# Kernel optimization log

Measured on AMD Instinct MI355X. Metric: run time of the kernel, lower is better.

Reference implementation:

```python
import jax, jax.numpy as jnp
import numpy as np

EPS = 1e-6
DIAG_SIZE = 128  # triu band half-width (init kwarg diag_size)
NEG_INF = -1e9


def feature_map(x):
    # tanh feature map: phi(x) = tanh(x) + 1 (positive feature map)
    return jnp.tanh(x) + 1.0


def causal_dot_product(Q, K, V):
    # Q,K: [N,L,H,E], V: [N,L,H,D]
    # running KV state: S_l = sum_{s<=l} K_s V_s^T, materialized via cumsum
    kv = jnp.cumsum(jnp.einsum('nlhe,nlhd->nlhed', K, V), axis=1)  # [N,L,H,E,D]
    return jnp.einsum('nlhe,nlhed->nlhd', Q, kv)


def setup_inputs() -> dict:
    key = jax.random.key(0)
    k1, k2, k3 = jax.random.split(key, 3)
    N, L, H, E = 2, 2048, 8, 64
    queries = jax.random.normal(k1, (N, L, H, E), dtype=jnp.float32)
    keys = jax.random.normal(k2, (N, L, H, E), dtype=jnp.float32)
    values = jax.random.normal(k3, (N, L, H, E), dtype=jnp.float32)
    key_lengths_mask = jnp.ones((N, L), dtype=jnp.float32)  # all keys valid
    blend = jnp.full((1,), 0.9, dtype=jnp.float32)  # learned blend param (init 0.9)
    return {"queries": queries, "keys": keys, "values": values,
            "key_lengths_mask": key_lengths_mask, "blend": blend}


def reference(queries, keys, values, key_lengths_mask, blend):
    N, L, H, E = queries.shape
    # ---- linear attention path (kernel_1 = tanh, kernel_2 = 'none') ----
    Q1 = feature_map(queries)
    K1 = feature_map(keys) * key_lengths_mask[:, :, None, None]
    Z1 = 1.0 / (jnp.einsum('nlhi,nlhi->nlh', Q1, jnp.cumsum(K1, axis=1)) + EPS)
    LV = causal_dot_product(Q1, K1, values) * Z1[..., None]  # [N,L,H,D]
    # ---- full softmax attention path (banded by triu) ----
    softmax_temp = 1.0 / np.sqrt(E).astype(np.float32)
    QK = jnp.einsum('nlhe,nshe->nhls', queries, keys)  # [N,H,L,L]
    l_idx = jnp.arange(L)[:, None]
    s_idx = jnp.arange(L)[None, :]
    causal_add = jnp.where(s_idx <= l_idx, 0.0, NEG_INF)  # lower-triangular mask
    key_add = jnp.where(key_lengths_mask > 0, 0.0, NEG_INF)  # [N,L]
    logits = softmax_temp * (QK + causal_add[None, None] + key_add[:, None, None, :])
    A = jax.nn.softmax(logits, axis=-1)
    # torch.triu(A, diagonal=-diag_size): keep s >= l - diag_size
    band = s_idx >= (l_idx - DIAG_SIZE)
    A = jnp.where(band[None, None], A, 0.0)
    # dropout: eval mode (identity)
    SV = jnp.einsum('nhls,nshd->nlhd', A, values)
    b = blend[0]
    return b * SV + (1.0 - b) * LV
```

## Files before the change

kernel.cpp:

```cpp
#include <hip/hip_runtime.h>
#include <math.h>

#define N_ 2
#define L_ 2048
#define H_ 8
#define E_ 64
#define D_ 64
#define C_ 128
#define NC (L_/C_)
#define ROWSTRIDE (H_*E_)
#define TEMP 0.125f
#define EPS_F 1e-6f
#define NEG_INF_F (-1e9f)
#define CHUNK_WS (E_*D_ + E_)
#define NCHUNKS (N_*H_*NC)
#define TPAD 136
#define PPAD 72

typedef __attribute__((ext_vector_type(8))) short short8;
typedef __attribute__((ext_vector_type(4))) float f32x4;

__device__ __forceinline__ short f2bf(float x) {
  unsigned u = __float_as_uint(x);
  u += 0x7fffu + ((u >> 16) & 1u);
  return (short)(u >> 16);
}
__device__ __forceinline__ float bf2f(short s) {
  return __uint_as_float(((unsigned)(unsigned short)s) << 16);
}
__device__ __forceinline__ float tanh1f(float x) {
  float e = __expf(-2.f * x);
  return 2.f * __builtin_amdgcn_rcpf(1.f + e);
}

__device__ __forceinline__ void load_bf16_tile(short* __restrict__ dst,
                                               const float* __restrict__ src) {
  const int t = threadIdx.x;
#pragma unroll
  for (int it = 0; it < 4; ++it) {
    int gi = it * 256 + t;
    int row = gi >> 3, g = gi & 7;
    const float* p = src + row * ROWSTRIDE + g * 8;
    float4 a = *(const float4*)p;
    float4 b = *(const float4*)(p + 4);
    short8 v;
    v[0] = f2bf(a.x); v[1] = f2bf(a.y); v[2] = f2bf(a.z); v[3] = f2bf(a.w);
    v[4] = f2bf(b.x); v[5] = f2bf(b.y); v[6] = f2bf(b.z); v[7] = f2bf(b.w);
    int sg = g ^ (row & 7);
    *(short8*)(dst + row * 64 + sg * 8) = v;
  }
}

__device__ __forceinline__ short8 frag_ld(const short* __restrict__ buf,
                                          int rowbase, int hf, int lane) {
  int r = rowbase + (lane & 15);
  int g = (hf * 4 + (lane >> 4)) ^ (r & 7);
  return *(const short8*)(buf + r * 64 + g * 8);
}
__device__ __forceinline__ short8 frag_ldT(const short* __restrict__ buf,
                                           int nbase, int g, int lane) {
  int r = nbase + (lane & 15);
  return *(const short8*)(buf + r * TPAD + g * 8);
}
__device__ __forceinline__ short8 frag_ldP(const short* __restrict__ buf,
                                           int rowbase, int ks, int lane) {
  int r = rowbase + (lane & 15);
  int g = ks * 4 + (lane >> 4);
  return *(const short8*)(buf + r * PPAD + g * 8);
}

extern "C" __global__ void __launch_bounds__(256, 4)
k_pre(const float* __restrict__ Q, const float* __restrict__ K,
      const float* __restrict__ V, const float* __restrict__ mask,
      float* __restrict__ ws, float* __restrict__ part) {
  __shared__ short ldsA[64 * TPAD];
  __shared__ short ldsB[64 * TPAD];
  __shared__ float fmsk[C_];
  const int orig = blockIdx.x;
  const int swz = (orig & 7) * 304 + (orig >> 3);
  const int t = threadIdx.x;
  const int w = t >> 6, lane = t & 63;
  const int col_lo = lane & 15;

  if (swz < 2176) {
    const int nh = swz / 136;
    const int p = swz - nh * 136;
    int qb = (int)((sqrtf(8.f * p + 1.f) - 1.f) * 0.5f);
    while ((qb + 1) * (qb + 2) / 2 <= p) ++qb;
    while (qb * (qb + 1) / 2 > p) --qb;
    const int kb = p - qb * (qb + 1) / 2;
    const int h = nh & (H_ - 1), n = nh >> 3;

    load_bf16_tile(ldsA, Q + ((n * L_ + qb * C_) * H_ + h) * E_);
    load_bf16_tile(ldsB, K + ((n * L_ + kb * C_) * H_ + h) * E_);
    if (t < C_) fmsk[t] = mask[n * L_ + kb * C_ + t];
    __syncthreads();

    const int rowbase = w * 32;
    short8 afr[2][2];
#pragma unroll
    for (int m = 0; m < 2; ++m)
#pragma unroll
      for (int hh = 0; hh < 2; ++hh)
        afr[m][hh] = frag_ld(ldsA, rowbase + 16 * m, hh, lane);

    f32x4 acc[2][8];
#pragma unroll
    for (int m = 0; m < 2; ++m)
#pragma unroll
      for (int c = 0; c < 8; ++c) acc[m][c] = (f32x4){0.f, 0.f, 0.f, 0.f};

#pragma unroll
    for (int c = 0; c < 8; ++c) {
      short8 b0 = frag_ld(ldsB, 16 * c, 0, lane);
      short8 b1 = frag_ld(ldsB, 16 * c, 1, lane);
#pragma unroll
      for (int m = 0; m < 2; ++m) {
        acc[m][c] = __builtin_amdgcn_mfma_f32_16x16x32_bf16(afr[m][0], b0, acc[m][c], 0, 0, 0);
        acc[m][c] = __builtin_amdgcn_mfma_f32_16x16x32_bf16(afr[m][1], b1, acc[m][c], 0, 0, 0);
      }
    }

    const bool diag = (kb == qb);
    float* pout = part + (size_t)(nh * NC + qb) * C_ * 16;
#pragma unroll
    for (int m = 0; m < 2; ++m) {
      const int rbase = rowbase + 16 * m + (lane >> 4) * 4;
      float rs[4] = {0.f, 0.f, 0.f, 0.f};
#pragma unroll
      for (int c = 0; c < 8; ++c) {
        const int col = 16 * c + col_lo;
        const float madd = (fmsk[col] > 0.f) ? 0.f : NEG_INF_F;
#pragma unroll
        for (int reg = 0; reg < 4; ++reg) {
          float x = acc[m][c][reg] + madd;
          if (diag && col > rbase + reg) x += NEG_INF_F;
          rs[reg] += __expf(x * TEMP);
        }
      }
#pragma unroll
      for (int off = 1; off < 16; off <<= 1) {
#pragma unroll
        for (int reg = 0; reg < 4; ++reg) rs[reg] += __shfl_xor(rs[reg], off);
      }
      if (col_lo == 0) {
#pragma unroll
        for (int reg = 0; reg < 4; ++reg) pout[(rbase + reg) * 16 + kb] = rs[reg];
      }
    }
  } else {
    const int id = swz - 2176;
    const int nh = id >> 4, c = id & 15;
    const int h = nh & (H_ - 1), n = nh >> 3;
    const int gbase = ((n * L_ + c * C_) * H_ + h) * E_;
    const int e = t & 63, sb = t >> 6;
    const int mbase = n * L_ + c * C_;
#pragma unroll
    for (int q = 0; q < 4; ++q) {
      int s0 = sb * 32 + q * 8;
      short8 kk, vv;
#pragma unroll
      for (int j = 0; j < 8; ++j) {
        float kx = K[gbase + (s0 + j) * ROWSTRIDE + e];
        kk[j] = f2bf(tanh1f(kx) * mask[mbase + s0 + j]);
        vv[j] = f2bf(V[gbase + (s0 + j) * ROWSTRIDE + e]);
      }
      *(short8*)(ldsA + e * TPAD + (s0 >> 3) * 8) = kk;
      *(short8*)(ldsB + e * TPAD + (s0 >> 3) * 8) = vv;
    }
    __syncthreads();

    f32x4 acc[4];
#pragma unroll
    for (int nn = 0; nn < 4; ++nn) acc[nn] = (f32x4){0.f, 0.f, 0.f, 0.f};
#pragma unroll
    for (int ks = 0; ks < 4; ++ks) {
      short8 a = frag_ldT(ldsB, 16 * w, ks * 4 + (lane >> 4), lane);
#pragma unroll
      for (int nn = 0; nn < 4; ++nn) {
        short8 b = frag_ldT(ldsA, 16 * nn, ks * 4 + (lane >> 4), lane);
        acc[nn] = __builtin_amdgcn_mfma_f32_16x16x32_bf16(a, b, acc[nn], 0, 0, 0);
      }
    }
    float* wsc = ws + (size_t)(nh * NC + c) * CHUNK_WS;
    const int drow = 16 * w + ((lane >> 4) << 2);
#pragma unroll
    for (int nn = 0; nn < 4; ++nn)
#pragma unroll
      for (int reg = 0; reg < 4; ++reg)
        wsc[(16 * nn + col_lo) * D_ + drow + reg] = acc[nn][reg];
    if (t < 64) {
      float s = 0.f;
#pragma unroll
      for (int g = 0; g < 16; ++g) {
        short8 v = *(const short8*)(ldsA + t * TPAD + g * 8);
#pragma unroll
        for (int j = 0; j < 8; ++j) s += bf2f(v[j]);
      }
      wsc[E_ * D_ + t] = s;
    }
  }
}

extern "C" __global__ void __launch_bounds__(256)
k_scan(float* __restrict__ ws) {
  const int bid = blockIdx.x;
  const int swz = (bid & 7) * 34 + (bid >> 3);
  const int nh = swz / 17, seg = swz - nh * 17;
  const int idx = seg * 256 + threadIdx.x;
  if (idx >= CHUNK_WS) return;
  float* base = ws + (size_t)nh * NC * CHUNK_WS + idx;
  float v[NC];
#pragma unroll
  for (int c = 0; c < NC; ++c) v[c] = base[(size_t)c * CHUNK_WS];
  float acc = 0.f;
#pragma unroll
  for (int c = 0; c < NC; ++c) {
    base[(size_t)c * CHUNK_WS] = acc;
    acc += v[c];
  }
}

extern "C" __global__ void __launch_bounds__(256, 3)
k_fused(const float* __restrict__ Q, const float* __restrict__ K,
        const float* __restrict__ V, const float* __restrict__ mask,
        const float* __restrict__ blend, const float* __restrict__ ws,
        const float* __restrict__ part, float* __restrict__ out) {
  __shared__ short kbuf[C_ * 64];
  __shared__ short kv[64 * TPAD];
  __shared__ short pbuf[64 * PPAD];
  __shared__ float zlds[64];
  __shared__ float dinv[64];
  __shared__ float ksum[E_];
  __shared__ float kmskC[C_];
  __shared__ float kmskP[C_];

  const int orig = blockIdx.x;
  const int swz = (orig & 7) * 64 + (orig >> 3);
  const int rh = swz & 1, qb = (swz >> 1) & (NC - 1), nh = swz >> 5;
  const int h = nh & (H_ - 1), n = nh >> 3;
  const int t = threadIdx.x;
  const int w = t >> 6, lane = t & 63;
  const int rowbase = w * 16;
  const int col_lo = lane & 15;
  const int rb = rowbase + ((lane >> 4) << 2);
  const int rtile0 = rh * 64 + rb;
  const int qgbase = ((n * L_ + qb * C_ + rh * 64) * H_ + h) * E_;
  const int kbase_chunk = ((n * L_ + qb * C_) * H_ + h) * E_;
  const float* wsc = ws + (size_t)(nh * NC + qb) * CHUNK_WS;
  const float bl = blend[0];
  const float ob = 1.f - bl;
  const int d = t & 63, sb = t >> 6;
  const bool haveprev = (qb > 0);
  const int kgp = ((n * L_ + (qb - 1) * C_) * H_ + h) * E_;

  float4 qraw[2][2];
  {
    const float* qp = Q + qgbase + (rowbase + (lane & 15)) * ROWSTRIDE;
#pragma unroll
    for (int kh = 0; kh < 2; ++kh) {
      int c0 = (kh * 4 + (lane >> 4)) * 8;
      qraw[kh][0] = *(const float4*)(qp + c0);
      qraw[kh][1] = *(const float4*)(qp + c0 + 4);
    }
  }
  short8 kraw[4];
  {
    const float* mrow = mask + n * L_ + qb * C_;
#pragma unroll
    for (int it = 0; it < 4; ++it) {
      int gi = it * 256 + t, row = gi >> 3, g = gi & 7;
      const float* p = K + kbase_chunk + row * ROWSTRIDE + g * 8;
      float4 a = *(const float4*)p, b = *(const float4*)(p + 4);
      float km = mrow[row];
      float xs[8] = {a.x, a.y, a.z, a.w, b.x, b.y, b.z, b.w};
      short8 vr, v1;
#pragma unroll
      for (int j = 0; j < 8; ++j) { vr[j] = f2bf(xs[j]); v1[j] = f2bf(tanh1f(xs[j]) * km); }
      kraw[it] = vr;
      *(short8*)(kbuf + row * 64 + (g ^ (row & 7)) * 8) = v1;
    }
  }
  {
    int eb = t >> 6;
#pragma unroll
    for (int q = 0; q < 2; ++q) {
      int e0 = eb * 16 + q * 8;
      short8 v;
#pragma unroll
      for (int j = 0; j < 8; ++j) v[j] = f2bf(wsc[(e0 + j) * D_ + d]);
      *(short8*)(kv + d * TPAD + (e0 >> 3) * 8) = v;
    }
  }
  short8 vcur[4];
#pragma unroll
  for (int q = 0; q < 4; ++q) {
#pragma unroll
    for (int j = 0; j < 8; ++j)
      vcur[q][j] = f2bf(V[kbase_chunk + (sb * 32 + q * 8 + j) * ROWSTRIDE + d]);
  }
  if (t < 64) {
    ksum[t] = wsc[E_ * D_ + t];
    const float* pb = part + ((size_t)(nh * NC + qb) * C_ + rh * 64 + t) * 16;
    float4 a = *(const float4*)pb, b = *(const float4*)(pb + 4);
    float4 c = *(const float4*)(pb + 8), d4 = *(const float4*)(pb + 12);
    float vv[16] = {a.x, a.y, a.z, a.w, b.x, b.y, b.z, b.w,
                    c.x, c.y, c.z, c.w, d4.x, d4.y, d4.z, d4.w};
    float s = 0.f;
#pragma unroll
    for (int j = 0; j < 16; ++j) s += (j <= qb) ? vv[j] : 0.f;
    dinv[t] = 1.f / s;
  }
  if (t < C_) {
    kmskC[t] = mask[n * L_ + qb * C_ + t];
    kmskP[t] = haveprev ? mask[n * L_ + (qb - 1) * C_ + t] : 1.f;
  }
  __syncthreads();

  short8 af1[2], afs[2];
#pragma unroll
  for (int kh = 0; kh < 2; ++kh) {
    float xs[8] = {qraw[kh][0].x, qraw[kh][0].y, qraw[kh][0].z, qraw[kh][0].w,
                   qraw[kh][1].x, qraw[kh][1].y, qraw[kh][1].z, qraw[kh][1].w};
#pragma unroll
    for (int j = 0; j < 8; ++j) { afs[kh][j] = f2bf(xs[j]); af1[kh][j] = f2bf(tanh1f(xs[j])); }
  }
  f32x4 c1[8];
#pragma unroll
  for (int ct = 0; ct < 8; ++ct) c1[ct] = (f32x4){0.f, 0.f, 0.f, 0.f};
#pragma unroll
  for (int ct = 0; ct < 8; ++ct) {
    short8 b0 = frag_ld(kbuf, 16 * ct, 0, lane);
    short8 b1 = frag_ld(kbuf, 16 * ct, 1, lane);
    c1[ct] = __builtin_amdgcn_mfma_f32_16x16x32_bf16(af1[0], b0, c1[ct], 0, 0, 0);
    c1[ct] = __builtin_amdgcn_mfma_f32_16x16x32_bf16(af1[1], b1, c1[ct], 0, 0, 0);
  }
  {
    float zz = 0.f;
#pragma unroll
    for (int kh = 0; kh < 2; ++kh) {
      int cb = (kh * 4 + (lane >> 4)) * 8;
#pragma unroll
      for (int j = 0; j < 8; ++j) zz += bf2f(af1[kh][j]) * ksum[cb + j];
    }
    zz += __shfl_xor(zz, 16);
    zz += __shfl_xor(zz, 32);
    if (lane < 16) zlds[rowbase + lane] = zz;
  }
  float rs[4] = {0.f, 0.f, 0.f, 0.f};
#pragma unroll
  for (int ct = 0; ct < 8; ++ct) {
    int col = 16 * ct + col_lo;
#pragma unroll
    for (int reg = 0; reg < 4; ++reg) {
      if (col <= rtile0 + reg) rs[reg] += c1[ct][reg];
      else c1[ct][reg] = 0.f;
    }
  }
#pragma unroll
  for (int off = 1; off < 16; off <<= 1)
#pragma unroll
    for (int reg = 0; reg < 4; ++reg) rs[reg] += __shfl_xor(rs[reg], off);

  f32x4 accL[4];
#pragma unroll
  for (int nn = 0; nn < 4; ++nn) accL[nn] = (f32x4){0.f, 0.f, 0.f, 0.f};
#pragma unroll
  for (int ks = 0; ks < 2; ++ks) {
    short8 bf[4];
#pragma unroll
    for (int nn = 0; nn < 4; ++nn)
      bf[nn] = frag_ldT(kv, 16 * nn, ks * 4 + (lane >> 4), lane);
#pragma unroll
    for (int nn = 0; nn < 4; ++nn)
      accL[nn] = __builtin_amdgcn_mfma_f32_16x16x32_bf16(af1[ks], bf[nn], accL[nn], 0, 0, 0);
  }
  __syncthreads();

#pragma unroll
  for (int it = 0; it < 4; ++it) {
    int gi = it * 256 + t, row = gi >> 3, g = gi & 7;
    *(short8*)(kbuf + row * 64 + (g ^ (row & 7)) * 8) = kraw[it];
  }
#pragma unroll
  for (int q = 0; q < 4; ++q)
    *(short8*)(kv + d * TPAD + ((sb * 32 + q * 8) >> 3) * 8) = vcur[q];
  __syncthreads();

  short8 pk[4], pv[4];
  if (haveprev) {
#pragma unroll
    for (int it = 0; it < 4; ++it) {
      int gi = it * 256 + t, row = gi >> 3, g = gi & 7;
      const float* p = K + kgp + row * ROWSTRIDE + g * 8;
      float4 a = *(const float4*)p, b = *(const float4*)(p + 4);
      float xs[8] = {a.x, a.y, a.z, a.w, b.x, b.y, b.z, b.w};
#pragma unroll
      for (int j = 0; j < 8; ++j) pk[it][j] = f2bf(xs[j]);
    }
#pragma unroll
    for (int q = 0; q < 4; ++q)
#pragma unroll
      for (int j = 0; j < 8; ++j)
        pv[q][j] = f2bf(V[kgp + (sb * 32 + q * 8 + j) * ROWSTRIDE + d]);
  }
#pragma unroll
  for (int hh = 0; hh < 2; ++hh) {
#pragma unroll
    for (int ch = 0; ch < 4; ++ch) {
      int ct = 4 * hh + ch, colh = 16 * ch + col_lo;
#pragma unroll
      for (int reg = 0; reg < 4; ++reg)
        pbuf[(rb + reg) * PPAD + colh] = f2bf(c1[ct][reg]);
    }
#pragma unroll
    for (int ks = 0; ks < 2; ++ks) {
      short8 ap = frag_ldP(pbuf, rowbase, ks, lane);
      short8 bv[4];
#pragma unroll
      for (int nn = 0; nn < 4; ++nn)
        bv[nn] = frag_ldT(kv, 16 * nn, 8 * hh + ks * 4 + (lane >> 4), lane);
#pragma unroll
      for (int nn = 0; nn < 4; ++nn)
        accL[nn] = __builtin_amdgcn_mfma_f32_16x16x32_bf16(ap, bv[nn], accL[nn], 0, 0, 0);
    }
  }
  f32x4 accS[4];
#pragma unroll
  for (int nn = 0; nn < 4; ++nn) accS[nn] = (f32x4){0.f, 0.f, 0.f, 0.f};
  {
    f32x4 cs[8];
#pragma unroll
    for (int ct = 0; ct < 8; ++ct) cs[ct] = (f32x4){0.f, 0.f, 0.f, 0.f};
#pragma unroll
    for (int ct = 0; ct < 8; ++ct) {
      short8 b0 = frag_ld(kbuf, 16 * ct, 0, lane);
      short8 b1 = frag_ld(kbuf, 16 * ct, 1, lane);
      cs[ct] = __builtin_amdgcn_mfma_f32_16x16x32_bf16(afs[0], b0, cs[ct], 0, 0, 0);
      cs[ct] = __builtin_amdgcn_mfma_f32_16x16x32_bf16(afs[1], b1, cs[ct], 0, 0, 0);
    }
#pragma unroll
    for (int ct = 0; ct < 8; ++ct) {
      int col = 16 * ct + col_lo;
      float madd = (kmskC[col] > 0.f) ? 0.f : NEG_INF_F;
#pragma unroll
      for (int reg = 0; reg < 4; ++reg) {
        float x = cs[ct][reg] + madd;
        if (col > rtile0 + reg) x += NEG_INF_F;
        cs[ct][reg] = __expf(x * TEMP);
      }
    }
#pragma unroll
    for (int hh = 0; hh < 2; ++hh) {
#pragma unroll
      for (int ch = 0; ch < 4; ++ch) {
        int ct = 4 * hh + ch, colh = 16 * ch + col_lo;
#pragma unroll
        for (int reg = 0; reg < 4; ++reg)
          pbuf[(rb + reg) * PPAD + colh] = f2bf(cs[ct][reg]);
      }
#pragma unroll
      for (int ks = 0; ks < 2; ++ks) {
        short8 ap = frag_ldP(pbuf, rowbase, ks, lane);
        short8 bv[4];
#pragma unroll
        for (int nn = 0; nn < 4; ++nn)
          bv[nn] = frag_ldT(kv, 16 * nn, 8 * hh + ks * 4 + (lane >> 4), lane);
#pragma unroll
        for (int nn = 0; nn < 4; ++nn)
          accS[nn] = __builtin_amdgcn_mfma_f32_16x16x32_bf16(ap, bv[nn], accS[nn], 0, 0, 0);
      }
    }
  }

  if (haveprev) {
    __syncthreads();
#pragma unroll
    for (int it = 0; it < 4; ++it) {
      int gi = it * 256 + t, row = gi >> 3, g = gi & 7;
      *(short8*)(kbuf + row * 64 + (g ^ (row & 7)) * 8) = pk[it];
    }
#pragma unroll
    for (int q = 0; q < 4; ++q)
      *(short8*)(kv + d * TPAD + ((sb * 32 + q * 8) >> 3) * 8) = pv[q];
    __syncthreads();

    f32x4 cs[8];
#pragma unroll
    for (int ct = 0; ct < 8; ++ct) cs[ct] = (f32x4){0.f, 0.f, 0.f, 0.f};
#pragma unroll
    for (int ct = 0; ct < 8; ++ct) {
      short8 b0 = frag_ld(kbuf, 16 * ct, 0, lane);
      short8 b1 = frag_ld(kbuf, 16 * ct, 1, lane);
      cs[ct] = __builtin_amdgcn_mfma_f32_16x16x32_bf16(afs[0], b0, cs[ct], 0, 0, 0);
      cs[ct] = __builtin_amdgcn_mfma_f32_16x16x32_bf16(afs[1], b1, cs[ct], 0, 0, 0);
    }
#pragma unroll
    for (int ct = 0; ct < 8; ++ct) {
      int col = 16 * ct + col_lo;
      float madd = (kmskP[col] > 0.f) ? 0.f : NEG_INF_F;
#pragma unroll
      for (int reg = 0; reg < 4; ++reg) {
        float x = cs[ct][reg] + madd;
        float pp = __expf(x * TEMP);
        if (col < rtile0 + reg) pp = 0.f;
        cs[ct][reg] = pp;
      }
    }
#pragma unroll
    for (int hh = 0; hh < 2; ++hh) {
#pragma unroll
      for (int ch = 0; ch < 4; ++ch) {
        int ct = 4 * hh + ch, colh = 16 * ch + col_lo;
#pragma unroll
        for (int reg = 0; reg < 4; ++reg)
          pbuf[(rb + reg) * PPAD + colh] = f2bf(cs[ct][reg]);
      }
#pragma unroll
      for (int ks = 0; ks < 2; ++ks) {
        short8 ap = frag_ldP(pbuf, rowbase, ks, lane);
        short8 bv[4];
#pragma unroll
        for (int nn = 0; nn < 4; ++nn)
          bv[nn] = frag_ldT(kv, 16 * nn, 8 * hh + ks * 4 + (lane >> 4), lane);
#pragma unroll
        for (int nn = 0; nn < 4; ++nn)
          accS[nn] = __builtin_amdgcn_mfma_f32_16x16x32_bf16(ap, bv[nn], accS[nn], 0, 0, 0);
      }
    }
  }

  float zrf[4], sdv[4];
#pragma unroll
  for (int reg = 0; reg < 4; ++reg) {
    zrf[reg] = ob / (zlds[rb + reg] + rs[reg] + EPS_F);
    sdv[reg] = bl * dinv[rb + reg];
  }
#pragma unroll
  for (int nn = 0; nn < 4; ++nn)
#pragma unroll
    for (int reg = 0; reg < 4; ++reg)
      out[qgbase + (rb + reg) * ROWSTRIDE + 16 * nn + col_lo] =
          zrf[reg] * accL[nn][reg] + sdv[reg] * accS[nn][reg];
}

extern "C" void kernel_launch(void* const* d_in, const int* in_sizes, int n_in,
                              void* d_out, int out_size, void* d_ws, size_t ws_size,
                              hipStream_t stream) {
  (void)in_sizes; (void)n_in; (void)out_size; (void)ws_size;
  const float* Q = (const float*)d_in[0];
  const float* K = (const float*)d_in[1];
  const float* V = (const float*)d_in[2];
  const float* mask = (const float*)d_in[3];
  const float* blend = (const float*)d_in[4];
  float* out = (float*)d_out;
  float* ws = (float*)d_ws;
  float* part = ws + (size_t)NCHUNKS * CHUNK_WS;

  k_pre<<<dim3(2432), dim3(256), 0, stream>>>(Q, K, V, mask, ws, part);
  k_scan<<<dim3(272), dim3(256), 0, stream>>>(ws);
  k_fused<<<dim3(N_ * H_ * NC * 2), dim3(256), 0, stream>>>(Q, K, V, mask, blend, ws, part, out);
}
```

Baseline: 52.86 us.

## Merge linear and softmax accumulators and defer loads to cut register pressure

The linear-attention and softmax accumulators are merged into one accumulator by folding the normalisation factors (zrf, blend*dinv) into the probabilities before each MFMA. Raw K/V/Q values are no longer held in registers across phases; they are re-read from global memory when needed. Launch bounds rise from 3 to 4 blocks per CU. The aim is higher occupancy from fewer live registers. In exchange there are extra global loads of Q, K and V, the previous chunk is no longer prefetched so its load latency is exposed, and intermediates are scaled before bf16 rounding.

```diff
diff --git a/kernel.cpp b/kernel.cpp
--- a/kernel.cpp
+++ b/kernel.cpp
@@ -125,7 +125,7 @@
     float* pout = part + (size_t)(nh * NC + qb) * C_ * 16;
 #pragma unroll
     for (int m = 0; m < 2; ++m) {
-      const int rbase = rowbase + 16 * m + (lane >> 4) * 4;
+      const int rbase = rowbase + 16 * m + ((lane >> 4) << 2);
       float rs[4] = {0.f, 0.f, 0.f, 0.f};
 #pragma unroll
       for (int c = 0; c < 8; ++c) {
@@ -221,7 +221,7 @@
   }
 }
 
-extern "C" __global__ void __launch_bounds__(256, 3)
+extern "C" __global__ void __launch_bounds__(256, 4)
 k_fused(const float* __restrict__ Q, const float* __restrict__ K,
         const float* __restrict__ V, const float* __restrict__ mask,
         const float* __restrict__ blend, const float* __restrict__ ws,
@@ -232,8 +232,8 @@
   __shared__ float zlds[64];
   __shared__ float dinv[64];
   __shared__ float ksum[E_];
-  __shared__ float kmskC[C_];
-  __shared__ float kmskP[C_];
+  __shared__ float kmC[C_];
+  __shared__ float kmP[C_];
 
   const int orig = blockIdx.x;
   const int swz = (orig & 7) * 64 + (orig >> 3);
@@ -254,17 +254,6 @@
   const bool haveprev = (qb > 0);
   const int kgp = ((n * L_ + (qb - 1) * C_) * H_ + h) * E_;
 
-  float4 qraw[2][2];
-  {
-    const float* qp = Q + qgbase + (rowbase + (lane & 15)) * ROWSTRIDE;
-#pragma unroll
-    for (int kh = 0; kh < 2; ++kh) {
-      int c0 = (kh * 4 + (lane >> 4)) * 8;
-      qraw[kh][0] = *(const float4*)(qp + c0);
-      qraw[kh][1] = *(const float4*)(qp + c0 + 4);
-    }
-  }
-  short8 kraw[4];
   {
     const float* mrow = mask + n * L_ + qb * C_;
 #pragma unroll
@@ -274,10 +263,9 @@
       float4 a = *(const float4*)p, b = *(const float4*)(p + 4);
       float km = mrow[row];
       float xs[8] = {a.x, a.y, a.z, a.w, b.x, b.y, b.z, b.w};
-      short8 vr, v1;
-#pragma unroll
-      for (int j = 0; j < 8; ++j) { vr[j] = f2bf(xs[j]); v1[j] = f2bf(tanh1f(xs[j]) * km); }
-      kraw[it] = vr;
+      short8 v1;
+#pragma unroll
+      for (int j = 0; j < 8; ++j) v1[j] = f2bf(tanh1f(xs[j]) * km);
       *(short8*)(kbuf + row * 64 + (g ^ (row & 7)) * 8) = v1;
     }
   }
@@ -291,13 +279,6 @@
       for (int j = 0; j < 8; ++j) v[j] = f2bf(wsc[(e0 + j) * D_ + d]);
       *(short8*)(kv + d * TPAD + (e0 >> 3) * 8) = v;
     }
-  }
-  short8 vcur[4];
-#pragma unroll
-  for (int q = 0; q < 4; ++q) {
-#pragma unroll
-    for (int j = 0; j < 8; ++j)
-      vcur[q][j] = f2bf(V[kbase_chunk + (sb * 32 + q * 8 + j) * ROWSTRIDE + d]);
   }
   if (t < 64) {
     ksum[t] = wsc[E_ * D_ + t];
@@ -312,18 +293,23 @@
     dinv[t] = 1.f / s;
   }
   if (t < C_) {
-    kmskC[t] = mask[n * L_ + qb * C_ + t];
-    kmskP[t] = haveprev ? mask[n * L_ + (qb - 1) * C_ + t] : 1.f;
+    kmC[t] = mask[n * L_ + qb * C_ + t];
+    kmP[t] = haveprev ? mask[n * L_ + (qb - 1) * C_ + t] : 1.f;
   }
   __syncthreads();
 
-  short8 af1[2], afs[2];
-#pragma unroll
-  for (int kh = 0; kh < 2; ++kh) {
-    float xs[8] = {qraw[kh][0].x, qraw[kh][0].y, qraw[kh][0].z, qraw[kh][0].w,
-                   qraw[kh][1].x, qraw[kh][1].y, qraw[kh][1].z, qraw[kh][1].w};
-#pragma unroll
-    for (int j = 0; j < 8; ++j) { afs[kh][j] = f2bf(xs[j]); af1[kh][j] = f2bf(tanh1f(xs[j])); }
+  short8 af1[2];
+  {
+    const float* qp = Q + qgbase + (rowbase + (lane & 15)) * ROWSTRIDE;
+#pragma unroll
+    for (int kh = 0; kh < 2; ++kh) {
+      int c0 = (kh * 4 + (lane >> 4)) * 8;
+      float4 a = *(const float4*)(qp + c0);
+      float4 b = *(const float4*)(qp + c0 + 4);
+      float xs[8] = {a.x, a.y, a.z, a.w, b.x, b.y, b.z, b.w};
+#pragma unroll
+      for (int j = 0; j < 8; ++j) af1[kh][j] = f2bf(tanh1f(xs[j]));
+    }
   }
   f32x4 c1[8];
 #pragma unroll
@@ -362,9 +348,9 @@
 #pragma unroll
     for (int reg = 0; reg < 4; ++reg) rs[reg] += __shfl_xor(rs[reg], off);
 
-  f32x4 accL[4];
-#pragma unroll
-  for (int nn = 0; nn < 4; ++nn) accL[nn] = (f32x4){0.f, 0.f, 0.f, 0.f};
+  f32x4 accO[4];
+#pragma unroll
+  for (int nn = 0; nn < 4; ++nn) accO[nn] = (f32x4){0.f, 0.f, 0.f, 0.f};
 #pragma unroll
   for (int ks = 0; ks < 2; ++ks) {
     short8 bf[4];
@@ -373,81 +359,173 @@
       bf[nn] = frag_ldT(kv, 16 * nn, ks * 4 + (lane >> 4), lane);
 #pragma unroll
     for (int nn = 0; nn < 4; ++nn)
-      accL[nn] = __builtin_amdgcn_mfma_f32_16x16x32_bf16(af1[ks], bf[nn], accL[nn], 0, 0, 0);
-  }
+      accO[nn] = __builtin_amdgcn_mfma_f32_16x16x32_bf16(af1[ks], bf[nn], accO[nn], 0, 0, 0);
+  }
+  float zrf[4], sdv[4];
+#pragma unroll
+  for (int reg = 0; reg < 4; ++reg) {
+    zrf[reg] = ob / (zlds[rb + reg] + rs[reg] + EPS_F);
+    sdv[reg] = bl * dinv[rb + reg];
+  }
+#pragma unroll
+  for (int nn = 0; nn < 4; ++nn)
+#pragma unroll
+    for (int reg = 0; reg < 4; ++reg) accO[nn][reg] *= zrf[reg];
+#pragma unroll
+  for (int ct = 0; ct < 8; ++ct)
+#pragma unroll
+    for (int reg = 0; reg < 4; ++reg) c1[ct][reg] *= zrf[reg];
   __syncthreads();
 
 #pragma unroll
   for (int it = 0; it < 4; ++it) {
     int gi = it * 256 + t, row = gi >> 3, g = gi & 7;
-    *(short8*)(kbuf + row * 64 + (g ^ (row & 7)) * 8) = kraw[it];
-  }
-#pragma unroll
-  for (int q = 0; q < 4; ++q)
-    *(short8*)(kv + d * TPAD + ((sb * 32 + q * 8) >> 3) * 8) = vcur[q];
+    const float* p = K + kbase_chunk + row * ROWSTRIDE + g * 8;
+    float4 a = *(const float4*)p, b = *(const float4*)(p + 4);
+    short8 v;
+    v[0] = f2bf(a.x); v[1] = f2bf(a.y); v[2] = f2bf(a.z); v[3] = f2bf(a.w);
+    v[4] = f2bf(b.x); v[5] = f2bf(b.y); v[6] = f2bf(b.z); v[7] = f2bf(b.w);
+    *(short8*)(kbuf + row * 64 + (g ^ (row & 7)) * 8) = v;
+  }
+#pragma unroll
+  for (int q = 0; q < 4; ++q) {
+    int s0 = sb * 32 + q * 8;
+    short8 v;
+#pragma unroll
+    for (int j = 0; j < 8; ++j) v[j] = f2bf(V[kbase_chunk + (s0 + j) * ROWSTRIDE + d]);
+    *(short8*)(kv + d * TPAD + (s0 >> 3) * 8) = v;
+  }
   __syncthreads();
 
-  short8 pk[4], pv[4];
+#pragma unroll
+  for (int hh = 0; hh < 2; ++hh) {
+#pragma unroll
+    for (int ch = 0; ch < 4; ++ch) {
+      int ct = 4 * hh + ch, colh = 16 * ch + col_lo;
+#pragma unroll
+      for (int reg = 0; reg < 4; ++reg)
+        pbuf[(rb + reg) * PPAD + colh] = f2bf(c1[ct][reg]);
+    }
+#pragma unroll
+    for (int ks = 0; ks < 2; ++ks) {
+      short8 ap = frag_ldP(pbuf, rowbase, ks, lane);
+      short8 bv[4];
+#pragma unroll
+      for (int nn = 0; nn < 4; ++nn)
+        bv[nn] = frag_ldT(kv, 16 * nn, 8 * hh + ks * 4 + (lane >> 4), lane);
+#pragma unroll
+      for (int nn = 0; nn < 4; ++nn)
+        accO[nn] = __builtin_amdgcn_mfma_f32_16x16x32_bf16(ap, bv[nn], accO[nn], 0, 0, 0);
+    }
+  }
+
+  {
+    short8 afs[2];
+    const float* qp = Q + qgbase + (rowbase + (lane & 15)) * ROWSTRIDE;
+#pragma unroll
+    for (int kh = 0; kh < 2; ++kh) {
+      int c0 = (kh * 4 + (lane >> 4)) * 8;
+      float4 a = *(const float4*)(qp + c0);
+      float4 b = *(const float4*)(qp + c0 + 4);
+      float xs[8] = {a.x, a.y, a.z, a.w, b.x, b.y, b.z, b.w};
+#pragma unroll
+      for (int j = 0; j < 8; ++j) afs[kh][j] = f2bf(xs[j]);
+    }
+#pragma unroll
+    for (int ct = 0; ct < 8; ++ct) c1[ct] = (f32x4){0.f, 0.f, 0.f, 0.f};
+#pragma unroll
+    for (int ct = 0; ct < 8; ++ct) {
+      short8 b0 = frag_ld(kbuf, 16 * ct, 0, lane);
+      short8 b1 = frag_ld(kbuf, 16 * ct, 1, lane);
+      c1[ct] = __builtin_amdgcn_mfma_f32_16x16x32_bf16(afs[0], b0, c1[ct], 0, 0, 0);
+      c1[ct] = __builtin_amdgcn_mfma_f32_16x16x32_bf16(afs[1], b1, c1[ct], 0, 0, 0);
+    }
+#pragma unroll
+    for (int ct = 0; ct < 8; ++ct) {
+      int col = 16 * ct + col_lo;
+      float madd = (kmC[col] > 0.f) ? 0.f : NEG_INF_F;
+#pragma unroll
+      for (int reg = 0; reg < 4; ++reg) {
+        float x = c1[ct][reg] + madd;
+        if (col > rtile0 + reg) x += NEG_INF_F;
+        c1[ct][reg] = sdv[reg] * __expf(x * TEMP);
+      }
+    }
+#pragma unroll
+    for (int hh = 0; hh < 2; ++hh) {
+#pragma unroll
+      for (int ch = 0; ch < 4; ++ch) {
+        int ct = 4 * hh + ch, colh = 16 * ch + col_lo;
+#pragma unroll
+        for (int reg = 0; reg < 4; ++reg)
+          pbuf[(rb + reg) * PPAD + colh] = f2bf(c1[ct][reg]);
+      }
+#pragma unroll
+      for (int ks = 0; ks < 2; ++ks) {
+        short8 ap = frag_ldP(pbuf, rowbase, ks, lane);
+        short8 bv[4];
+#pragma unroll
+        for (int nn = 0; nn < 4; ++nn)
+          bv[nn] = frag_ldT(kv, 16 * nn, 8 * hh + ks * 4 + (lane >> 4), lane);
+#pragma unroll
+        for (int nn = 0; nn < 4; ++nn)
+          accO[nn] = __builtin_amdgcn_mfma_f32_16x16x32_bf16(ap, bv[nn], accO[nn], 0, 0, 0);
+      }
+    }
+  }
+
   if (haveprev) {
+    __syncthreads();
 #pragma unroll
     for (int it = 0; it < 4; ++it) {
       int gi = it * 256 + t, row = gi >> 3, g = gi & 7;
       const float* p = K + kgp + row * ROWSTRIDE + g * 8;
       float4 a = *(const float4*)p, b = *(const float4*)(p + 4);
+      short8 v;
+      v[0] = f2bf(a.x); v[1] = f2bf(a.y); v[2] = f2bf(a.z); v[3] = f2bf(a.w);
+      v[4] = f2bf(b.x); v[5] = f2bf(b.y); v[6] = f2bf(b.z); v[7] = f2bf(b.w);
+      *(short8*)(kbuf + row * 64 + (g ^ (row & 7)) * 8) = v;
+    }
+#pragma unroll
+    for (int q = 0; q < 4; ++q) {
+      int s0 = sb * 32 + q * 8;
+      short8 v;
+#pragma unroll
+      for (int j = 0; j < 8; ++j) v[j] = f2bf(V[kgp + (s0 + j) * ROWSTRIDE + d]);
+      *(short8*)(kv + d * TPAD + (s0 >> 3) * 8) = v;
+    }
+    __syncthreads();
+
+    short8 afs[2];
+    const float* qp = Q + qgbase + (rowbase + (lane & 15)) * ROWSTRIDE;
+#pragma unroll
+    for (int kh = 0; kh < 2; ++kh) {
+      int c0 = (kh * 4 + (lane >> 4)) * 8;
+      float4 a = *(const float4*)(qp + c0);
+      float4 b = *(const float4*)(qp + c0 + 4);
       float xs[8] = {a.x, a.y, a.z, a.w, b.x, b.y, b.z, b.w};
 #pragma unroll
-      for (int j = 0; j < 8; ++j) pk[it][j] = f2bf(xs[j]);
-    }
-#pragma unroll
-    for (int q = 0; q < 4; ++q)
-#pragma unroll
-      for (int j = 0; j < 8; ++j)
-        pv[q][j] = f2bf(V[kgp + (sb * 32 + q * 8 + j) * ROWSTRIDE + d]);
-  }
-#pragma unroll
-  for (int hh = 0; hh < 2; ++hh) {
-#pragma unroll
-    for (int ch = 0; ch < 4; ++ch) {
-      int ct = 4 * hh + ch, colh = 16 * ch + col_lo;
-#pragma unroll
-      for (int reg = 0; reg < 4; ++reg)
-        pbuf[(rb + reg) * PPAD + colh] = f2bf(c1[ct][reg]);
-    }
-#pragma unroll
-    for (int ks = 0; ks < 2; ++ks) {
-      short8 ap = frag_ldP(pbuf, rowbase, ks, lane);
-      short8 bv[4];
-#pragma unroll
-      for (int nn = 0; nn < 4; ++nn)
-        bv[nn] = frag_ldT(kv, 16 * nn, 8 * hh + ks * 4 + (lane >> 4), lane);
-#pragma unroll
-      for (int nn = 0; nn < 4; ++nn)
-        accL[nn] = __builtin_amdgcn_mfma_f32_16x16x32_bf16(ap, bv[nn], accL[nn], 0, 0, 0);
-    }
-  }
-  f32x4 accS[4];
-#pragma unroll
-  for (int nn = 0; nn < 4; ++nn) accS[nn] = (f32x4){0.f, 0.f, 0.f, 0.f};
-  {
-    f32x4 cs[8];
-#pragma unroll
-    for (int ct = 0; ct < 8; ++ct) cs[ct] = (f32x4){0.f, 0.f, 0.f, 0.f};
+      for (int j = 0; j < 8; ++j) afs[kh][j] = f2bf(xs[j]);
+    }
+#pragma unroll
+    for (int ct = 0; ct < 8; ++ct) c1[ct] = (f32x4){0.f, 0.f, 0.f, 0.f};
 #pragma unroll
     for (int ct = 0; ct < 8; ++ct) {
       short8 b0 = frag_ld(kbuf, 16 * ct, 0, lane);
       short8 b1 = frag_ld(kbuf, 16 * ct, 1, lane);
-      cs[ct] = __builtin_amdgcn_mfma_f32_16x16x32_bf16(afs[0], b0, cs[ct], 0, 0, 0);
-      cs[ct] = __builtin_amdgcn_mfma_f32_16x16x32_bf16(afs[1], b1, cs[ct], 0, 0, 0);
+      c1[ct] = __builtin_amdgcn_mfma_f32_16x16x32_bf16(afs[0], b0, c1[ct], 0, 0, 0);
+      c1[ct] = __builtin_amdgcn_mfma_f32_16x16x32_bf16(afs[1], b1, c1[ct], 0, 0, 0);
     }
 #pragma unroll
     for (int ct = 0; ct < 8; ++ct) {
       int col = 16 * ct + col_lo;
-      float madd = (kmskC[col] > 0.f) ? 0.f : NEG_INF_F;
+      float madd = (kmP[col] > 0.f) ? 0.f : NEG_INF_F;
 #pragma unroll
       for (int reg = 0; reg < 4; ++reg) {
-        float x = cs[ct][reg] + madd;
-        if (col > rtile0 + reg) x += NEG_INF_F;
-        cs[ct][reg] = __expf(x * TEMP);
+        float x = c1[ct][reg] + madd;
+        float pp = sdv[reg] * __expf(x * TEMP);
+        if (col < rtile0 + reg) pp = 0.f;
+        c1[ct][reg] = pp;
       }
     }
 #pragma unroll
@@ -457,7 +535,7 @@
         int ct = 4 * hh + ch, colh = 16 * ch + col_lo;
 #pragma unroll
         for (int reg = 0; reg < 4; ++reg)
-          pbuf[(rb + reg) * PPAD + colh] = f2bf(cs[ct][reg]);
+          pbuf[(rb + reg) * PPAD + colh] = f2bf(c1[ct][reg]);
       }
 #pragma unroll
       for (int ks = 0; ks < 2; ++ks) {
@@ -468,80 +546,16 @@
           bv[nn] = frag_ldT(kv, 16 * nn, 8 * hh + ks * 4 + (lane >> 4), lane);
 #pragma unroll
         for (int nn = 0; nn < 4; ++nn)
-          accS[nn] = __builtin_amdgcn_mfma_f32_16x16x32_bf16(ap, bv[nn], accS[nn], 0, 0, 0);
-      }
-    }
-  }
-
-  if (haveprev) {
-    __syncthreads();
-#pragma unroll
-    for (int it = 0; it < 4; ++it) {
-      int gi = it * 256 + t, row = gi >> 3, g = gi & 7;
-      *(short8*)(kbuf + row * 64 + (g ^ (row & 7)) * 8) = pk[it];
-    }
-#pragma unroll
-    for (int q = 0; q < 4; ++q)
-      *(short8*)(kv + d * TPAD + ((sb * 32 + q * 8) >> 3) * 8) = pv[q];
-    __syncthreads();
-
-    f32x4 cs[8];
-#pragma unroll
-    for (int ct = 0; ct < 8; ++ct) cs[ct] = (f32x4){0.f, 0.f, 0.f, 0.f};
-#pragma unroll
-    for (int ct = 0; ct < 8; ++ct) {
-      short8 b0 = frag_ld(kbuf, 16 * ct, 0, lane);
-      short8 b1 = frag_ld(kbuf, 16 * ct, 1, lane);
-      cs[ct] = __builtin_amdgcn_mfma_f32_16x16x32_bf16(afs[0], b0, cs[ct], 0, 0, 0);
-      cs[ct] = __builtin_amdgcn_mfma_f32_16x16x32_bf16(afs[1], b1, cs[ct], 0, 0, 0);
-    }
-#pragma unroll
-    for (int ct = 0; ct < 8; ++ct) {
-      int col = 16 * ct + col_lo;
-      float madd = (kmskP[col] > 0.f) ? 0.f : NEG_INF_F;
-#pragma unroll
-      for (int reg = 0; reg < 4; ++reg) {
-        float x = cs[ct][reg] + madd;
-        float pp = __expf(x * TEMP);
-        if (col < rtile0 + reg) pp = 0.f;
-        cs[ct][reg] = pp;
-      }
-    }
-#pragma unroll
-    for (int hh = 0; hh < 2; ++hh) {
-#pragma unroll
-      for (int ch = 0; ch < 4; ++ch) {
-        int ct = 4 * hh + ch, colh = 16 * ch + col_lo;
-#pragma unroll
-        for (int reg = 0; reg < 4; ++reg)
-          pbuf[(rb + reg) * PPAD + colh] = f2bf(cs[ct][reg]);
-      }
-#pragma unroll
-      for (int ks = 0; ks < 2; ++ks) {
-        short8 ap = frag_ldP(pbuf, rowbase, ks, lane);
-        short8 bv[4];
-#pragma unroll
-        for (int nn = 0; nn < 4; ++nn)
-          bv[nn] = frag_ldT(kv, 16 * nn, 8 * hh + ks * 4 + (lane >> 4), lane);
-#pragma unroll
-        for (int nn = 0; nn < 4; ++nn)
-          accS[nn] = __builtin_amdgcn_mfma_f32_16x16x32_bf16(ap, bv[nn], accS[nn], 0, 0, 0);
-      }
-    }
-  }
-
-  float zrf[4], sdv[4];
-#pragma unroll
-  for (int reg = 0; reg < 4; ++reg) {
-    zrf[reg] = ob / (zlds[rb + reg] + rs[reg] + EPS_F);
-    sdv[reg] = bl * dinv[rb + reg];
-  }
+          accO[nn] = __builtin_amdgcn_mfma_f32_16x16x32_bf16(ap, bv[nn], accO[nn], 0, 0, 0);
+      }
+    }
+  }
+
 #pragma unroll
   for (int nn = 0; nn < 4; ++nn)
 #pragma unroll
     for (int reg = 0; reg < 4; ++reg)
-      out[qgbase + (rb + reg) * ROWSTRIDE + 16 * nn + col_lo] =
-          zrf[reg] * accL[nn][reg] + sdv[reg] * accS[nn][reg];
+      out[qgbase + (rb + reg) * ROWSTRIDE + 16 * nn + col_lo] = accO[nn][reg];
 }
 
 extern "C" void kernel_launch(void* const* d_in, const int* in_sizes, int n_in,
```

Result: faster. 47.59 us (-10.0%).
